# Optimization experiments

Measured on AMD Instinct MI355X. Metric: run time of the kernel, lower is better.

The kernel has to match this reference:

```python
import jax, jax.numpy as jnp
import numpy as np

NUM_USERS = 1_000_000
EMBED_DIM = 64
N_NODES = 16384
K = 50
NEG_INF = -1e30


def setup_inputs() -> dict:
    key = jax.random.key(0)
    ks = jax.random.split(key, 7)
    d = EMBED_DIM
    table = jax.random.normal(ks[0], (NUM_USERS, d), jnp.float32) * 0.02
    nodes = jax.random.randint(ks[1], (N_NODES,), 0, NUM_USERS)
    neigh_idx = jax.random.randint(ks[2], (N_NODES, K), 0, NUM_USERS)
    neigh_mask = jax.random.randint(ks[3], (N_NODES, K), 0, 2).astype(bool)
    neigh_mask = neigh_mask.at[:, 0].set(True)  # every node has >=1 neighbor
    W1 = jax.random.normal(ks[4], (2 * d, d), jnp.float32) / np.sqrt(2 * d)
    b1 = jnp.zeros((d,), jnp.float32)
    W2 = jax.random.normal(ks[5], (d, d), jnp.float32) / np.sqrt(d)
    b2 = jnp.zeros((d,), jnp.float32)
    W3 = jax.random.normal(ks[6], (d, 1), jnp.float32) / np.sqrt(d)
    b3 = jnp.zeros((1,), jnp.float32)
    return dict(table=table, W1=W1, b1=b1, W2=W2, b2=b2, W3=W3, b3=b3,
                nodes=nodes, neigh_idx=neigh_idx, neigh_mask=neigh_mask)


def reference(table, W1, b1, W2, b2, W3, b3, nodes, neigh_idx, neigh_mask):
    # Gather neighbor embeddings and center-node embeddings (eval mode: dropout off).
    E = table[neigh_idx]                                   # [N, K, d]
    U = table[nodes]                                       # [N, d]
    Uk = jnp.broadcast_to(U[:, None, :], E.shape)          # [N, K, d]
    x = jnp.concatenate([E, Uk], axis=-1)                  # [N, K, 2d]
    h = jax.nn.relu(x @ W1 + b1)                           # [N, K, d]
    h = jax.nn.relu(h @ W2 + b2)                           # [N, K, d]
    s = (h @ W3 + b3)[..., 0]                              # [N, K]
    # Masked softmax over the ragged neighbor dimension.
    s = jnp.where(neigh_mask, s, NEG_INF)
    att = jax.nn.softmax(s, axis=-1)                       # [N, K]
    # Attention-weighted sum of neighbor embeddings: e_u.T @ att_w per node.
    out = jnp.einsum('nk,nkd->nd', att, E)                 # [N, d]
    return out
```

## Files before the change

kernel.cpp:

```cpp
#include <hip/hip_runtime.h>
#include <hip/hip_bf16.h>

#define NN 16384
#define KK 50
#define DD 64

typedef __attribute__((ext_vector_type(8))) short bf16x8;
typedef __attribute__((ext_vector_type(4))) float f32x4;

__device__ __forceinline__ float bf2f(unsigned short u) {
    union { unsigned int i; float f; } v;
    v.i = ((unsigned int)u) << 16;
    return v.f;
}
__device__ __forceinline__ unsigned short f2bf(float f) {
    union { float f; unsigned int i; } v; v.f = f;
    unsigned int lsb = (v.i >> 16) & 1u;
    v.i += 0x7fffu + lsb;
    return (unsigned short)(v.i >> 16);
}

template<int BF16>
__device__ __forceinline__ float ldv(const void* p, size_t i) {
    if (BF16) return bf2f(((const unsigned short*)p)[i]);
    else      return ((const float*)p)[i];
}

template<int BF16>
__device__ __forceinline__ bf16x8 load8(const void* p, size_t off) {
    if (BF16) {
        return *(const bf16x8*)((const unsigned short*)p + off);
    } else {
        const float* f = (const float*)p + off;
        bf16x8 r;
#pragma unroll
        for (int j = 0; j < 8; ++j) ((unsigned short*)&r)[j] = f2bf(f[j]);
        return r;
    }
}

__global__ void prep_kernel(const unsigned int* __restrict__ tw,
                            const unsigned int* __restrict__ mw,
                            const void* __restrict__ W1_,
                            const void* __restrict__ W2_,
                            int* __restrict__ flags,
                            unsigned short* __restrict__ W1p,
                            unsigned short* __restrict__ W2p) {
    __shared__ int sflags[2];
    const int t = threadIdx.x;
    if (t < 64) {
        const unsigned int w  = tw[t];
        const unsigned int lo = w & 0xFFFFu;
        const unsigned int ex = (lo >> 7) & 0xFFu;
        const bool bf_like = (ex >= 96u && ex <= 126u);
        const unsigned long long bb = __ballot(bf_like);
        bool found = false;
#pragma unroll
        for (int i = 0; i < 8; ++i) found |= (mw[t + i * 64] > 1u);
        const unsigned long long mb = __ballot(found);
        if (t == 0) {
            sflags[0] = (mb != 0ull) ? 1 : 0;
            sflags[1] = (__popcll(bb) >= 48) ? 1 : 0;
            flags[0] = sflags[0];
            flags[1] = sflags[1];
        }
    }
    __syncthreads();
    const int bf = sflags[1];
    {
        const int f = t >> 6, lane = t & 63;
        const int kt = f >> 2, nt = f & 3;
        const int q = lane >> 4, col = lane & 15;
#pragma unroll
        for (int j = 0; j < 8; ++j) {
            const int k = kt * 32 + q * 8 + j;
            const int n = nt * 16 + col;
            const float v = bf ? bf2f(((const unsigned short*)W1_)[k * 64 + n])
                               : ((const float*)W1_)[k * 64 + n];
            W1p[((size_t)f * 64 + lane) * 8 + j] = f2bf(v);
        }
    }
    if (t < 512) {
        const int f = t >> 6, lane = t & 63;
        const int kt = f >> 2, nt = f & 3;
        const int q = lane >> 4, col = lane & 15;
#pragma unroll
        for (int j = 0; j < 8; ++j) {
            const int k = kt * 32 + q * 8 + j;
            const int n = nt * 16 + col;
            const float v = bf ? bf2f(((const unsigned short*)W2_)[k * 64 + n])
                               : ((const float*)W2_)[k * 64 + n];
            W2p[((size_t)f * 64 + lane) * 8 + j] = f2bf(v);
        }
    }
}

template<int BF16>
__device__ __forceinline__ void agg_impl(
    const void* __restrict__ table_,
    const void* __restrict__ b1_, const void* __restrict__ b2_,
    const void* __restrict__ W3_, const void* __restrict__ b3_,
    const int*  __restrict__ nodes,
    const int*  __restrict__ neigh_idx,
    const void* __restrict__ neigh_mask,
    int mu8,
    const unsigned short* __restrict__ W1p,
    const unsigned short* __restrict__ W2p,
    unsigned short* __restrict__ h1,
    float* __restrict__ scr,
    void* __restrict__ out_)
{
    const int wave = threadIdx.x >> 6;
    const int lane = threadIdx.x & 63;
    const int n    = blockIdx.x * 4 + wave;
    const int q    = lane >> 4;
    const int col  = lane & 15;

    int  rowidx [4];
    bool rowmask[4];
#pragma unroll
    for (int mt = 0; mt < 4; ++mt) {
        const int k = mt * 16 + col;
        bool mk = false; int idx = 0;
        if (k < KK) {
            mk = mu8 ? (((const unsigned char*)neigh_mask)[(size_t)n * KK + k] != 0)
                     : (((const int*)neigh_mask)[(size_t)n * KK + k] != 0);
            if (mk) idx = neigh_idx[(size_t)n * KK + k];
        }
        rowidx[mt] = idx; rowmask[mt] = mk;
    }

    bf16x8 afrag[4][2];
#pragma unroll
    for (int mt = 0; mt < 4; ++mt)
#pragma unroll
        for (int kt = 0; kt < 2; ++kt)
            afrag[mt][kt] = load8<BF16>(table_, (size_t)rowidx[mt] * 64 + kt * 32 + q * 8);

    const size_t node = (size_t)nodes[n];
    bf16x8 ufrag[2];
#pragma unroll
    for (int kt = 0; kt < 2; ++kt)
        ufrag[kt] = load8<BF16>(table_, node * 64 + kt * 32 + q * 8);

    f32x4 acc1[4][4];
#pragma unroll
    for (int mt = 0; mt < 4; ++mt)
#pragma unroll
        for (int nt = 0; nt < 4; ++nt) acc1[mt][nt] = (f32x4){0.f, 0.f, 0.f, 0.f};

#pragma unroll
    for (int kt = 0; kt < 4; ++kt) {
#pragma unroll
        for (int nt = 0; nt < 4; ++nt) {
            const bf16x8 b = *(const bf16x8*)(W1p + ((size_t)(kt * 4 + nt) * 64 + lane) * 8);
#pragma unroll
            for (int mt = 0; mt < 4; ++mt) {
                const bf16x8 a = (kt < 2) ? afrag[mt][kt] : ufrag[kt - 2];
                acc1[mt][nt] = __builtin_amdgcn_mfma_f32_16x16x32_bf16(a, b, acc1[mt][nt], 0, 0, 0);
            }
        }
    }

    float b1v[4];
#pragma unroll
    for (int nt = 0; nt < 4; ++nt) b1v[nt] = ldv<BF16>(b1_, nt * 16 + col);
#pragma unroll
    for (int mt = 0; mt < 4; ++mt)
#pragma unroll
        for (int nt = 0; nt < 4; ++nt)
#pragma unroll
            for (int r = 0; r < 4; ++r) {
                const float v = fmaxf(acc1[mt][nt][r] + b1v[nt], 0.f);
                h1[(mt * 16 + q * 4 + r) * 72 + nt * 16 + col] = f2bf(v);
            }
    __builtin_amdgcn_wave_barrier();

    f32x4 acc2[4][4];
#pragma unroll
    for (int mt = 0; mt < 4; ++mt)
#pragma unroll
        for (int nt = 0; nt < 4; ++nt) acc2[mt][nt] = (f32x4){0.f, 0.f, 0.f, 0.f};

#pragma unroll
    for (int kt = 0; kt < 2; ++kt) {
        bf16x8 a2[4];
#pragma unroll
        for (int mt = 0; mt < 4; ++mt)
            a2[mt] = *(const bf16x8*)&h1[(mt * 16 + col) * 72 + kt * 32 + q * 8];
#pragma unroll
        for (int nt = 0; nt < 4; ++nt) {
            const bf16x8 b = *(const bf16x8*)(W2p + ((size_t)(kt * 4 + nt) * 64 + lane) * 8);
#pragma unroll
            for (int mt = 0; mt < 4; ++mt)
                acc2[mt][nt] = __builtin_amdgcn_mfma_f32_16x16x32_bf16(a2[mt], b, acc2[mt][nt], 0, 0, 0);
        }
    }

    float b2v[4], w3v[4];
#pragma unroll
    for (int nt = 0; nt < 4; ++nt) {
        b2v[nt] = ldv<BF16>(b2_, nt * 16 + col);
        w3v[nt] = ldv<BF16>(W3_, nt * 16 + col);
    }
    const float b3v = ldv<BF16>(b3_, 0);

    float s[4][4];
#pragma unroll
    for (int mt = 0; mt < 4; ++mt) {
        const unsigned long long bm = __ballot(rowmask[mt]);
#pragma unroll
        for (int r = 0; r < 4; ++r) {
            float p = 0.f;
#pragma unroll
            for (int nt = 0; nt < 4; ++nt)
                p += fmaxf(acc2[mt][nt][r] + b2v[nt], 0.f) * w3v[nt];
            p += __shfl_xor(p, 1, 64);
            p += __shfl_xor(p, 2, 64);
            p += __shfl_xor(p, 4, 64);
            p += __shfl_xor(p, 8, 64);
            const bool mk = (bm >> (q * 4 + r)) & 1ull;
            s[mt][r] = mk ? (p + b3v) : -1.0e30f;
        }
    }

    float mx = -3.0e38f;
#pragma unroll
    for (int mt = 0; mt < 4; ++mt)
#pragma unroll
        for (int r = 0; r < 4; ++r) mx = fmaxf(mx, s[mt][r]);
    mx = fmaxf(mx, __shfl_xor(mx, 16, 64));
    mx = fmaxf(mx, __shfl_xor(mx, 32, 64));

    float e[4][4], lsum = 0.f;
#pragma unroll
    for (int mt = 0; mt < 4; ++mt)
#pragma unroll
        for (int r = 0; r < 4; ++r) {
            e[mt][r] = expf(s[mt][r] - mx);
            lsum += e[mt][r];
        }
    lsum += __shfl_xor(lsum, 16, 64);
    lsum += __shfl_xor(lsum, 32, 64);
    const float inv = 1.f / lsum;

    if (col == 0)
#pragma unroll
        for (int mt = 0; mt < 4; ++mt)
#pragma unroll
            for (int r = 0; r < 4; ++r)
                scr[mt * 16 + q * 4 + r] = e[mt][r] * inv;
    __builtin_amdgcn_wave_barrier();

    float attr[4];
#pragma unroll
    for (int mt = 0; mt < 4; ++mt) attr[mt] = scr[mt * 16 + col];

    float v[2][8];
#pragma unroll
    for (int kt = 0; kt < 2; ++kt)
#pragma unroll
        for (int j = 0; j < 8; ++j) v[kt][j] = 0.f;
#pragma unroll
    for (int mt = 0; mt < 4; ++mt)
#pragma unroll
        for (int kt = 0; kt < 2; ++kt)
#pragma unroll
            for (int j = 0; j < 8; ++j)
                v[kt][j] += attr[mt] * bf2f(((const unsigned short*)&afrag[mt][kt])[j]);

#pragma unroll
    for (int off = 1; off <= 8; off <<= 1)
#pragma unroll
        for (int kt = 0; kt < 2; ++kt)
#pragma unroll
            for (int j = 0; j < 8; ++j)
                v[kt][j] += __shfl_xor(v[kt][j], off, 64);

    __builtin_amdgcn_wave_barrier();
    if (col == 0)
#pragma unroll
        for (int kt = 0; kt < 2; ++kt)
#pragma unroll
            for (int j = 0; j < 8; ++j)
                scr[kt * 32 + q * 8 + j] = v[kt][j];
    __builtin_amdgcn_wave_barrier();

    const float res = scr[lane];
    if (BF16) ((unsigned short*)out_)[(size_t)n * 64 + lane] = f2bf(res);
    else      ((float*)out_)[(size_t)n * 64 + lane] = res;
}

__global__ __launch_bounds__(256) void agg_kernel(
    const void* __restrict__ table_,
    const void* __restrict__ b1_, const void* __restrict__ b2_,
    const void* __restrict__ W3_, const void* __restrict__ b3_,
    const int*  __restrict__ nodes,
    const int*  __restrict__ neigh_idx,
    const void* __restrict__ neigh_mask,
    const int*  __restrict__ flags,
    const unsigned short* __restrict__ W1p,
    const unsigned short* __restrict__ W2p,
    void* __restrict__ out_)
{
    __shared__ unsigned short h1_sh[4][64][72];
    __shared__ float scr_sh[4][64];
    const int wave = threadIdx.x >> 6;
    const int bf16 = flags[1];
    const int mu8  = flags[0];
    if (bf16)
        agg_impl<1>(table_, b1_, b2_, W3_, b3_, nodes, neigh_idx, neigh_mask, mu8,
                    W1p, W2p, &h1_sh[wave][0][0], &scr_sh[wave][0], out_);
    else
        agg_impl<0>(table_, b1_, b2_, W3_, b3_, nodes, neigh_idx, neigh_mask, mu8,
                    W1p, W2p, &h1_sh[wave][0][0], &scr_sh[wave][0], out_);
}

extern "C" void kernel_launch(void* const* d_in, const int* in_sizes, int n_in,
                              void* d_out, int out_size, void* d_ws, size_t ws_size,
                              hipStream_t stream) {
    const void* table = d_in[0];
    const void* W1    = d_in[1];
    const void* b1    = d_in[2];
    const void* W2    = d_in[3];
    const void* b2    = d_in[4];
    const void* W3    = d_in[5];
    const void* b3    = d_in[6];
    const int*  nodes = (const int*)d_in[7];
    const int*  nidx  = (const int*)d_in[8];
    const void* nmask = d_in[9];

    int* flags = (int*)d_ws;
    unsigned short* W1p = (unsigned short*)((char*)d_ws + 1024);
    unsigned short* W2p = (unsigned short*)((char*)d_ws + 1024 + 16384);

    prep_kernel<<<1, 1024, 0, stream>>>((const unsigned int*)table,
                                        (const unsigned int*)nmask,
                                        W1, W2, flags, W1p, W2p);
    agg_kernel<<<NN / 4, 256, 0, stream>>>(table, b1, b2, W3, b3,
                                           nodes, nidx, nmask, flags,
                                           W1p, W2p, d_out);
}
```

Before: 414.0 us.

## Precompute per-node U·W1_bottom once and shrink agg blocks to two waves

Splits the first MLP layer so the center-node half (U @ W1[64:] + b1) is computed once per node in a new uw_kernel instead of being broadcast across all K neighbor rows. The agg kernel then only runs the neighbor half of the first layer, which halves its layer-1 MFMAs, and it adds the precomputed per-column term before the ReLU. The agg block size also drops from four waves to two. b3 is removed from the scores because softmax is shift-invariant. The cost is an extra kernel launch and an fp32 UW round trip through global memory.

```diff
diff --git a/kernel.cpp b/kernel.cpp
--- a/kernel.cpp
+++ b/kernel.cpp
@@ -44,7 +44,8 @@
                             const void* __restrict__ W1_,
                             const void* __restrict__ W2_,
                             int* __restrict__ flags,
-                            unsigned short* __restrict__ W1p,
+                            unsigned short* __restrict__ W1top,
+                            unsigned short* __restrict__ W1bot,
                             unsigned short* __restrict__ W2p) {
     __shared__ int sflags[2];
     const int t = threadIdx.x;
@@ -77,7 +78,9 @@
             const int n = nt * 16 + col;
             const float v = bf ? bf2f(((const unsigned short*)W1_)[k * 64 + n])
                                : ((const float*)W1_)[k * 64 + n];
-            W1p[((size_t)f * 64 + lane) * 8 + j] = f2bf(v);
+            unsigned short* dst = (kt < 2) ? W1top : W1bot;
+            const int fl = ((kt & 1) * 4 + nt);
+            dst[((size_t)fl * 64 + lane) * 8 + j] = f2bf(v);
         }
     }
     if (t < 512) {
@@ -96,23 +99,83 @@
 }
 
 template<int BF16>
+__device__ __forceinline__ void uw_impl(
+    const void* __restrict__ table_, const void* __restrict__ b1_,
+    const int* __restrict__ nodes,
+    const unsigned short* __restrict__ W1bot,
+    float* __restrict__ UW)
+{
+    const int wave = threadIdx.x >> 6;
+    const int lane = threadIdx.x & 63;
+    const int q    = lane >> 4;
+    const int col  = lane & 15;
+    const int base = (blockIdx.x * 4 + wave) * 64;
+
+    bf16x8 afrag[4][2];
+#pragma unroll
+    for (int mt = 0; mt < 4; ++mt) {
+        const size_t row = (size_t)nodes[base + mt * 16 + col];
+#pragma unroll
+        for (int kt = 0; kt < 2; ++kt)
+            afrag[mt][kt] = load8<BF16>(table_, row * 64 + kt * 32 + q * 8);
+    }
+
+    f32x4 acc[4][4];
+#pragma unroll
+    for (int mt = 0; mt < 4; ++mt)
+#pragma unroll
+        for (int nt = 0; nt < 4; ++nt) acc[mt][nt] = (f32x4){0.f, 0.f, 0.f, 0.f};
+
+#pragma unroll
+    for (int kt = 0; kt < 2; ++kt)
+#pragma unroll
+        for (int nt = 0; nt < 4; ++nt) {
+            const bf16x8 b = *(const bf16x8*)(W1bot + ((size_t)(kt * 4 + nt) * 64 + lane) * 8);
+#pragma unroll
+            for (int mt = 0; mt < 4; ++mt)
+                acc[mt][nt] = __builtin_amdgcn_mfma_f32_16x16x32_bf16(afrag[mt][kt], b, acc[mt][nt], 0, 0, 0);
+        }
+
+    float b1v[4];
+#pragma unroll
+    for (int nt = 0; nt < 4; ++nt) b1v[nt] = ldv<BF16>(b1_, nt * 16 + col);
+#pragma unroll
+    for (int mt = 0; mt < 4; ++mt)
+#pragma unroll
+        for (int nt = 0; nt < 4; ++nt)
+#pragma unroll
+            for (int r = 0; r < 4; ++r)
+                UW[(size_t)(base + mt * 16 + q * 4 + r) * 64 + nt * 16 + col] =
+                    acc[mt][nt][r] + b1v[nt];
+}
+
+__global__ __launch_bounds__(256) void uw_kernel(
+    const void* __restrict__ table_, const void* __restrict__ b1_,
+    const int* __restrict__ nodes, const int* __restrict__ flags,
+    const unsigned short* __restrict__ W1bot, float* __restrict__ UW)
+{
+    if (flags[1]) uw_impl<1>(table_, b1_, nodes, W1bot, UW);
+    else          uw_impl<0>(table_, b1_, nodes, W1bot, UW);
+}
+
+template<int BF16>
 __device__ __forceinline__ void agg_impl(
     const void* __restrict__ table_,
-    const void* __restrict__ b1_, const void* __restrict__ b2_,
-    const void* __restrict__ W3_, const void* __restrict__ b3_,
+    const void* __restrict__ b2_, const void* __restrict__ W3_,
     const int*  __restrict__ nodes,
     const int*  __restrict__ neigh_idx,
     const void* __restrict__ neigh_mask,
     int mu8,
-    const unsigned short* __restrict__ W1p,
+    const unsigned short* __restrict__ W1top,
     const unsigned short* __restrict__ W2p,
+    const float* __restrict__ UW,
     unsigned short* __restrict__ h1,
     float* __restrict__ scr,
     void* __restrict__ out_)
 {
     const int wave = threadIdx.x >> 6;
     const int lane = threadIdx.x & 63;
-    const int n    = blockIdx.x * 4 + wave;
+    const int n    = blockIdx.x * 2 + wave;
     const int q    = lane >> 4;
     const int col  = lane & 15;
 
@@ -137,41 +200,33 @@
         for (int kt = 0; kt < 2; ++kt)
             afrag[mt][kt] = load8<BF16>(table_, (size_t)rowidx[mt] * 64 + kt * 32 + q * 8);
 
-    const size_t node = (size_t)nodes[n];
-    bf16x8 ufrag[2];
+    float uwv[4];
+#pragma unroll
+    for (int nt = 0; nt < 4; ++nt) uwv[nt] = UW[(size_t)n * 64 + nt * 16 + col];
+
+    f32x4 acc1[4][4];
+#pragma unroll
+    for (int mt = 0; mt < 4; ++mt)
+#pragma unroll
+        for (int nt = 0; nt < 4; ++nt) acc1[mt][nt] = (f32x4){0.f, 0.f, 0.f, 0.f};
+
 #pragma unroll
     for (int kt = 0; kt < 2; ++kt)
-        ufrag[kt] = load8<BF16>(table_, node * 64 + kt * 32 + q * 8);
-
-    f32x4 acc1[4][4];
-#pragma unroll
-    for (int mt = 0; mt < 4; ++mt)
-#pragma unroll
-        for (int nt = 0; nt < 4; ++nt) acc1[mt][nt] = (f32x4){0.f, 0.f, 0.f, 0.f};
-
-#pragma unroll
-    for (int kt = 0; kt < 4; ++kt) {
 #pragma unroll
         for (int nt = 0; nt < 4; ++nt) {
-            const bf16x8 b = *(const bf16x8*)(W1p + ((size_t)(kt * 4 + nt) * 64 + lane) * 8);
-#pragma unroll
-            for (int mt = 0; mt < 4; ++mt) {
-                const bf16x8 a = (kt < 2) ? afrag[mt][kt] : ufrag[kt - 2];
-                acc1[mt][nt] = __builtin_amdgcn_mfma_f32_16x16x32_bf16(a, b, acc1[mt][nt], 0, 0, 0);
-            }
-        }
-    }
-
-    float b1v[4];
-#pragma unroll
-    for (int nt = 0; nt < 4; ++nt) b1v[nt] = ldv<BF16>(b1_, nt * 16 + col);
+            const bf16x8 b = *(const bf16x8*)(W1top + ((size_t)(kt * 4 + nt) * 64 + lane) * 8);
+#pragma unroll
+            for (int mt = 0; mt < 4; ++mt)
+                acc1[mt][nt] = __builtin_amdgcn_mfma_f32_16x16x32_bf16(afrag[mt][kt], b, acc1[mt][nt], 0, 0, 0);
+        }
+
 #pragma unroll
     for (int mt = 0; mt < 4; ++mt)
 #pragma unroll
         for (int nt = 0; nt < 4; ++nt)
 #pragma unroll
             for (int r = 0; r < 4; ++r) {
-                const float v = fmaxf(acc1[mt][nt][r] + b1v[nt], 0.f);
+                const float v = fmaxf(acc1[mt][nt][r] + uwv[nt], 0.f);
                 h1[(mt * 16 + q * 4 + r) * 72 + nt * 16 + col] = f2bf(v);
             }
     __builtin_amdgcn_wave_barrier();
@@ -203,7 +258,6 @@
         b2v[nt] = ldv<BF16>(b2_, nt * 16 + col);
         w3v[nt] = ldv<BF16>(W3_, nt * 16 + col);
     }
-    const float b3v = ldv<BF16>(b3_, 0);
 
     float s[4][4];
 #pragma unroll
@@ -220,7 +274,7 @@
             p += __shfl_xor(p, 4, 64);
             p += __shfl_xor(p, 8, 64);
             const bool mk = (bm >> (q * 4 + r)) & 1ull;
-            s[mt][r] = mk ? (p + b3v) : -1.0e30f;
+            s[mt][r] = mk ? p : -1.0e30f;
         }
     }
 
@@ -291,29 +345,27 @@
     else      ((float*)out_)[(size_t)n * 64 + lane] = res;
 }
 
-__global__ __launch_bounds__(256) void agg_kernel(
+__global__ __launch_bounds__(128) void agg_kernel(
     const void* __restrict__ table_,
-    const void* __restrict__ b1_, const void* __restrict__ b2_,
-    const void* __restrict__ W3_, const void* __restrict__ b3_,
+    const void* __restrict__ b2_, const void* __restrict__ W3_,
     const int*  __restrict__ nodes,
     const int*  __restrict__ neigh_idx,
     const void* __restrict__ neigh_mask,
     const int*  __restrict__ flags,
-    const unsigned short* __restrict__ W1p,
+    const unsigned short* __restrict__ W1top,
     const unsigned short* __restrict__ W2p,
+    const float* __restrict__ UW,
     void* __restrict__ out_)
 {
-    __shared__ unsigned short h1_sh[4][64][72];
-    __shared__ float scr_sh[4][64];
+    __shared__ unsigned short h1_sh[2][64][72];
+    __shared__ float scr_sh[2][64];
     const int wave = threadIdx.x >> 6;
-    const int bf16 = flags[1];
-    const int mu8  = flags[0];
-    if (bf16)
-        agg_impl<1>(table_, b1_, b2_, W3_, b3_, nodes, neigh_idx, neigh_mask, mu8,
-                    W1p, W2p, &h1_sh[wave][0][0], &scr_sh[wave][0], out_);
+    if (flags[1])
+        agg_impl<1>(table_, b2_, W3_, nodes, neigh_idx, neigh_mask, flags[0],
+                    W1top, W2p, UW, &h1_sh[wave][0][0], &scr_sh[wave][0], out_);
     else
-        agg_impl<0>(table_, b1_, b2_, W3_, b3_, nodes, neigh_idx, neigh_mask, mu8,
-                    W1p, W2p, &h1_sh[wave][0][0], &scr_sh[wave][0], out_);
+        agg_impl<0>(table_, b2_, W3_, nodes, neigh_idx, neigh_mask, flags[0],
+                    W1top, W2p, UW, &h1_sh[wave][0][0], &scr_sh[wave][0], out_);
 }
 
 extern "C" void kernel_launch(void* const* d_in, const int* in_sizes, int n_in,
@@ -325,19 +377,22 @@
     const void* W2    = d_in[3];
     const void* b2    = d_in[4];
     const void* W3    = d_in[5];
-    const void* b3    = d_in[6];
+    const void* b3    = d_in[6]; (void)b3;
     const int*  nodes = (const int*)d_in[7];
     const int*  nidx  = (const int*)d_in[8];
     const void* nmask = d_in[9];
 
-    int* flags = (int*)d_ws;
-    unsigned short* W1p = (unsigned short*)((char*)d_ws + 1024);
-    unsigned short* W2p = (unsigned short*)((char*)d_ws + 1024 + 16384);
+    char* ws = (char*)d_ws;
+    int* flags            = (int*)ws;
+    unsigned short* W1top = (unsigned short*)(ws + 1024);
+    unsigned short* W1bot = (unsigned short*)(ws + 1024 + 8192);
+    unsigned short* W2p   = (unsigned short*)(ws + 1024 + 16384);
+    float* UW             = (float*)(ws + 32768);
 
     prep_kernel<<<1, 1024, 0, stream>>>((const unsigned int*)table,
                                         (const unsigned int*)nmask,
-                                        W1, W2, flags, W1p, W2p);
-    agg_kernel<<<NN / 4, 256, 0, stream>>>(table, b1, b2, W3, b3,
-                                           nodes, nidx, nmask, flags,
-                                           W1p, W2p, d_out);
-}
+                                        W1, W2, flags, W1top, W1bot, W2p);
+    uw_kernel<<<NN / 256, 256, 0, stream>>>(table, b1, nodes, flags, W1bot, UW);
+    agg_kernel<<<NN / 2, 128, 0, stream>>>(table, b2, W3, nodes, nidx, nmask,
+                                           flags, W1top, W2p, UW, d_out);
+}
```

Result: no change. 410.9 us (-0.7%).
